# Kernel optimization log

Measured on AMD Instinct MI355X. Metric: run time of the kernel, lower is better.

Reference implementation:

```python
import jax, jax.numpy as jnp
import numpy as np

N, C, H, W = 64, 128, 32, 32
EPS = 1e-5


def _layernorm_chw(x, w, b):
    # LayerNorm over normalized_shape=(C,H,W): last 3 dims
    mu = jnp.mean(x, axis=(1, 2, 3), keepdims=True)
    var = jnp.var(x, axis=(1, 2, 3), keepdims=True)
    return (x - mu) * jax.lax.rsqrt(var + EPS) * w[None] + b[None]


def _conv1x1(x, w, b):
    # x: [N,C,H,W], w: [Cout,Cin], b: [Cout]
    return jnp.einsum('oc,nchw->nohw', w, x) + b[None, :, None, None]


def setup_inputs() -> dict:
    key = jax.random.key(0)
    ks = jax.random.split(key, 12)
    d = {
        'query': jax.random.normal(ks[0], (N, C, H, W), jnp.float32),
        'key': jax.random.normal(ks[1], (N, C, H, W), jnp.float32),
        'value': jax.random.normal(ks[2], (N, C, H, W), jnp.float32),
        'ln1_w': jnp.ones((C, H, W), jnp.float32),
        'ln1_b': jnp.zeros((C, H, W), jnp.float32),
        'ln2_w': jnp.ones((C, H, W), jnp.float32),
        'ln2_b': jnp.zeros((C, H, W), jnp.float32),
        'ln3_w': jnp.ones((C, H, W), jnp.float32),
        'ln3_b': jnp.zeros((C, H, W), jnp.float32),
        'wq': jax.random.normal(ks[3], (C, C), jnp.float32) / np.sqrt(C),
        'bq': jnp.zeros((C,), jnp.float32),
        'wk': jax.random.normal(ks[4], (C, C), jnp.float32) / np.sqrt(C),
        'bk': jnp.zeros((C,), jnp.float32),
        'wv': jax.random.normal(ks[5], (C, C), jnp.float32) / np.sqrt(C),
        'bv': jnp.zeros((C,), jnp.float32),
    }
    return d


def reference(query, key, value, ln1_w, ln1_b, ln2_w, ln2_b, ln3_w, ln3_b,
              wq, bq, wk, bk, wv, bv):
    qn = _layernorm_chw(query, ln1_w, ln1_b)  # residual uses normalized query
    kn = _layernorm_chw(key, ln2_w, ln2_b)
    vn = _layernorm_chw(value, ln3_w, ln3_b)
    q = _conv1x1(qn, wq, bq).reshape(N, C, H * W)
    k = _conv1x1(kn, wk, bk).reshape(N, C, H * W)
    v = _conv1x1(vn, wv, bv).reshape(N, C, H * W)
    # attention[n,i,j] = sum_c k[n,c,i] q[n,c,j] / sqrt(C); softmax over i (dim=1)
    attn = jnp.einsum('nci,ncj->nij', k, q) / jnp.sqrt(jnp.float32(C))
    attn = jax.nn.softmax(attn, axis=1)
    out = jnp.einsum('nci,nij->ncj', v, attn).reshape(N, C, H, W)
    x = qn + out
    return x.reshape(N, -1)  # flatten(start_dim=1)
```

## Files before the change

kernel.cpp:

```cpp
#include <hip/hip_runtime.h>


#define NS 64
#define CD 128
#define SD 1024
#define MEL (CD*SD)
#define SCALE 0.08838834764831845f

typedef __attribute__((ext_vector_type(4))) float floatx4;
typedef __attribute__((ext_vector_type(8))) short short8;
typedef __attribute__((ext_vector_type(4))) short short4v;

typedef __attribute__((address_space(1))) const void global_cvoid;
typedef __attribute__((address_space(3))) void lds_void;

__device__ __forceinline__ void gl16(const void* g, void* l) {
  __builtin_amdgcn_global_load_lds((global_cvoid*)g, (lds_void*)l, 16, 0, 0);
}
__device__ __forceinline__ unsigned short f2bf(float f) {
  union { float f; unsigned int i; } v; v.f = f;
  unsigned int i = v.i;
  return (unsigned short)((i + 0x7fffu + ((i >> 16) & 1u)) >> 16);
}
__device__ __forceinline__ unsigned int pkbf(float lo, float hi) {
  unsigned int r;
  asm("v_cvt_pk_bf16_f32 %0, %1, %2" : "=v"(r) : "v"(lo), "v"(hi));
  return r;
}
__device__ __forceinline__ short8 ld8_bf16(const float* __restrict__ p) {
  floatx4 a = *(const floatx4*)p;
  floatx4 b = *(const floatx4*)(p + 4);
  short8 r;
  r[0] = (short)f2bf(a[0]); r[1] = (short)f2bf(a[1]);
  r[2] = (short)f2bf(a[2]); r[3] = (short)f2bf(a[3]);
  r[4] = (short)f2bf(b[0]); r[5] = (short)f2bf(b[1]);
  r[6] = (short)f2bf(b[2]); r[7] = (short)f2bf(b[3]);
  return r;
}
__device__ __forceinline__ floatx4 mfma16(short8 a, short8 b, floatx4 c) {
  return __builtin_amdgcn_mfma_f32_16x16x32_bf16(a, b, c, 0, 0, 0);
}

__global__ __launch_bounds__(256) void stats_kernel(
    const float* __restrict__ q, const float* __restrict__ k,
    const float* __restrict__ v, float* __restrict__ sums)
{
  int b = blockIdx.x;
  int tn = b >> 3, part = b & 7;
  int t = tn >> 6;
  const float* x = (t == 0 ? q : (t == 1 ? k : v))
                 + (size_t)(tn & 63) * MEL + part * (MEL / 8);
  float s1 = 0.f, s2 = 0.f;
#pragma unroll
  for (int it = 0; it < 16; ++it) {
    floatx4 u = *(const floatx4*)(x + it * 1024 + threadIdx.x * 4);
#pragma unroll
    for (int j = 0; j < 4; ++j) { float f = u[j]; s1 += f; s2 += f * f; }
  }
#pragma unroll
  for (int off = 32; off; off >>= 1) {
    s1 += __shfl_xor(s1, off, 64);
    s2 += __shfl_xor(s2, off, 64);
  }
  if ((threadIdx.x & 63) == 0) {
    atomicAdd(&sums[tn], s1);
    atomicAdd(&sums[192 + tn], s2);
  }
}

__global__ __launch_bounds__(512, 4) void proj_kernel(
  const float* __restrict__ k, const float* __restrict__ v,
  const float* __restrict__ l2w, const float* __restrict__ l2b,
  const float* __restrict__ l3w, const float* __restrict__ l3b,
  const float* __restrict__ wk, const float* __restrict__ bk,
  const float* __restrict__ wv, const float* __restrict__ bv,
  const float* __restrict__ sums,
  unsigned short* __restrict__ kT, unsigned short* __restrict__ vN)
{
  int n  = blockIdx.x, t = blockIdx.y, st = blockIdx.z;
  const float* x  = (t == 0 ? k : v) + (size_t)n * MEL;
  const float* lw = (t == 0 ? l2w : l3w);
  const float* lb = (t == 0 ? l2b : l3b);
  const float* W  = (t == 0 ? wk : wv);
  const float* Bs = (t == 0 ? bk : bv);

  float mu  = sums[(t + 1) * 64 + n] * (1.f / MEL);
  float var = sums[192 + (t + 1) * 64 + n] * (1.f / MEL) - mu * mu;
  float rs  = rsqrtf(var + 1e-5f);
  float a_ln = rs, b_ln = -mu * rs;

  __shared__ __align__(16) unsigned short Xt[128 * 136];

  int tid = threadIdx.x;
  int cb = tid & 15, sb = (tid >> 4) & 15, half = tid >> 8;
  int s0 = st * 128;

  unsigned int w32[8][2];
#pragma unroll
  for (int pr = 0; pr < 2; ++pr) {
    int c0 = cb * 8 + half * 4 + pr * 2;
    const float* xp0 = x  + (size_t)c0 * SD + s0 + sb * 8;
    const float* wp0 = lw + (size_t)c0 * SD + s0 + sb * 8;
    const float* bp0 = lb + (size_t)c0 * SD + s0 + sb * 8;
    float xv0[8], xv1[8], wv0[8], wv1[8], bv0[8], bv1[8];
    *(floatx4*)xv0 = *(const floatx4*)xp0;       *(floatx4*)(xv0+4) = *(const floatx4*)(xp0+4);
    *(floatx4*)xv1 = *(const floatx4*)(xp0+SD);  *(floatx4*)(xv1+4) = *(const floatx4*)(xp0+SD+4);
    *(floatx4*)wv0 = *(const floatx4*)wp0;       *(floatx4*)(wv0+4) = *(const floatx4*)(wp0+4);
    *(floatx4*)wv1 = *(const floatx4*)(wp0+SD);  *(floatx4*)(wv1+4) = *(const floatx4*)(wp0+SD+4);
    *(floatx4*)bv0 = *(const floatx4*)bp0;       *(floatx4*)(bv0+4) = *(const floatx4*)(bp0+4);
    *(floatx4*)bv1 = *(const floatx4*)(bp0+SD);  *(floatx4*)(bv1+4) = *(const floatx4*)(bp0+SD+4);
#pragma unroll
    for (int js = 0; js < 8; ++js) {
      unsigned int lo = f2bf((xv0[js] * a_ln + b_ln) * wv0[js] + bv0[js]);
      unsigned int hi = f2bf((xv1[js] * a_ln + b_ln) * wv1[js] + bv1[js]);
      w32[js][pr] = lo | (hi << 16);
    }
  }
#pragma unroll
  for (int js = 0; js < 8; ++js) {
    unsigned int* d = (unsigned int*)&Xt[(sb * 8 + js) * 136 + cb * 8 + half * 4];
    d[0] = w32[js][0]; d[1] = w32[js][1];
  }
  __syncthreads();

  int lane = tid & 63, w = tid >> 6;
  int quad = lane >> 4, l16 = lane & 15;

  short8 Af[4];
#pragma unroll
  for (int kk = 0; kk < 4; ++kk)
    Af[kk] = ld8_bf16(W + (w * 16 + l16) * CD + kk * 32 + quad * 8);

  floatx4 acc[8];
  floatx4 zz = {0.f, 0.f, 0.f, 0.f};
#pragma unroll
  for (int nb = 0; nb < 8; ++nb) acc[nb] = zz;
#pragma unroll
  for (int kk = 0; kk < 4; ++kk)
#pragma unroll
    for (int nb = 0; nb < 8; ++nb) {
      short8 Bf = *(const short8*)&Xt[(nb * 16 + l16) * 136 + kk * 32 + quad * 8];
      acc[nb] = mfma16(Af[kk], Bf, acc[nb]);
    }

  float bsv[4];
#pragma unroll
  for (int r = 0; r < 4; ++r) bsv[r] = Bs[w * 16 + quad * 4 + r];

  if (t == 0) {
#pragma unroll
    for (int nb = 0; nb < 8; ++nb) {
      short4v pk;
#pragma unroll
      for (int r = 0; r < 4; ++r) pk[r] = (short)f2bf(acc[nb][r] + bsv[r]);
      size_t g = (size_t)n * MEL + (size_t)(s0 + nb * 16 + l16) * CD + w * 16 + quad * 4;
      *(short4v*)(kT + g) = pk;
    }
  } else {
#pragma unroll
    for (int nb = 0; nb < 8; ++nb)
#pragma unroll
      for (int r = 0; r < 4; ++r) {
        size_t g = (size_t)n * MEL + (size_t)(w * 16 + quad * 4 + r) * SD + s0 + nb * 16 + l16;
        vN[g] = f2bf(acc[nb][r] + bsv[r]);
      }
  }
}

__device__ __forceinline__ void stage_tile(
    const unsigned short* __restrict__ kbase0,
    const unsigned short* __restrict__ vbase0,
    char* smem, int ti, int buf, int w, int lane)
{
  const unsigned short* kb = kbase0 + (size_t)ti * 64 * CD;
  char* KD = smem + buf * 16384;
  char* VD = smem + 32768 + buf * 16384;
#pragma unroll
  for (int it = 0; it < 4; ++it) {
    int nch = w * 256 + it * 64 + lane;
    int i = nch >> 4, cc = nch & 15;
    int csrc = (cc & 8) | ((cc & 7) ^ (i & 7));
    gl16(kb + i * CD + csrc * 8, KD + (w * 256 + it * 64) * 16);
  }
#pragma unroll
  for (int it = 0; it < 4; ++it) {
    int nch = w * 256 + it * 64 + lane;
    int c = nch >> 3, ci = nch & 7;
    int isrc = ci ^ (c & 7);
    gl16(vbase0 + (size_t)c * SD + ti * 64 + isrc * 8, VD + (w * 256 + it * 64) * 16);
  }
}

__global__ __launch_bounds__(256, 2) void attn_kernel(
  const float* __restrict__ qraw, const float* __restrict__ l1w,
  const float* __restrict__ l1b, const float* __restrict__ wq,
  const float* __restrict__ bq,
  const unsigned short* __restrict__ kT, const unsigned short* __restrict__ vN,
  const float* __restrict__ sums, float* __restrict__ out)
{
  int n = blockIdx.x, jt = blockIdx.y;
  int j0 = jt * 128;

  __shared__ __align__(16) char smem[65536];
  unsigned short* Xt = (unsigned short*)smem;

  int tid = threadIdx.x, lane = tid & 63, w = tid >> 6;
  int quad = lane >> 4, l16 = lane & 15;

  float mu  = sums[n] * (1.f / MEL);
  float var = sums[192 + n] * (1.f / MEL) - mu * mu;
  float rsd = rsqrtf(var + 1e-5f);
  float a_ln = rsd, b_ln = -mu * rsd;
  const float* qb = qraw + (size_t)n * MEL;

  {
    int cb = tid & 15, sb = tid >> 4;
    unsigned int w32[8][4];
#pragma unroll
    for (int pr = 0; pr < 4; ++pr) {
      int c0 = cb * 8 + pr * 2;
      const float* xp0 = qb  + (size_t)c0 * SD + j0 + sb * 8;
      const float* wp0 = l1w + (size_t)c0 * SD + j0 + sb * 8;
      const float* bp0 = l1b + (size_t)c0 * SD + j0 + sb * 8;
      float xv0[8], xv1[8], wv0[8], wv1[8], bv0[8], bv1[8];
      *(floatx4*)xv0 = *(const floatx4*)xp0;       *(floatx4*)(xv0+4) = *(const floatx4*)(xp0+4);
      *(floatx4*)xv1 = *(const floatx4*)(xp0+SD);  *(floatx4*)(xv1+4) = *(const floatx4*)(xp0+SD+4);
      *(floatx4*)wv0 = *(const floatx4*)wp0;       *(floatx4*)(wv0+4) = *(const floatx4*)(wp0+4);
      *(floatx4*)wv1 = *(const floatx4*)(wp0+SD);  *(floatx4*)(wv1+4) = *(const floatx4*)(wp0+SD+4);
      *(floatx4*)bv0 = *(const floatx4*)bp0;       *(floatx4*)(bv0+4) = *(const floatx4*)(bp0+4);
      *(floatx4*)bv1 = *(const floatx4*)(bp0+SD);  *(floatx4*)(bv1+4) = *(const floatx4*)(bp0+SD+4);
#pragma unroll
      for (int js = 0; js < 8; ++js) {
        unsigned int lo = f2bf((xv0[js] * a_ln + b_ln) * wv0[js] + bv0[js]);
        unsigned int hi = f2bf((xv1[js] * a_ln + b_ln) * wv1[js] + bv1[js]);
        w32[js][pr] = lo | (hi << 16);
      }
    }
#pragma unroll
    for (int js = 0; js < 8; ++js)
      *(floatx4*)&Xt[(sb * 8 + js) * 136 + cb * 8] = *(floatx4*)w32[js];
  }
  __syncthreads();

  floatx4 zz = {0.f, 0.f, 0.f, 0.f};
  {
    short8 Af[2][4];
#pragma unroll
    for (int mi = 0; mi < 2; ++mi)
#pragma unroll
      for (int kk = 0; kk < 4; ++kk)
        Af[mi][kk] = ld8_bf16(wq + ((w * 2 + mi) * 16 + l16) * CD + kk * 32 + quad * 8);
    floatx4 accq[2][8];
#pragma unroll
    for (int mi = 0; mi < 2; ++mi)
#pragma unroll
      for (int nb = 0; nb < 8; ++nb) accq[mi][nb] = zz;
#pragma unroll
    for (int kk = 0; kk < 4; ++kk)
#pragma unroll
      for (int nb = 0; nb < 8; ++nb) {
        short8 Bf = *(const short8*)&Xt[(nb * 16 + l16) * 136 + kk * 32 + quad * 8];
        accq[0][nb] = mfma16(Af[0][kk], Bf, accq[0][nb]);
        accq[1][nb] = mfma16(Af[1][kk], Bf, accq[1][nb]);
      }
    __syncthreads();
    float bqs[2][4];
#pragma unroll
    for (int mi = 0; mi < 2; ++mi)
#pragma unroll
      for (int r = 0; r < 4; ++r) bqs[mi][r] = bq[(w * 2 + mi) * 16 + quad * 4 + r];
#pragma unroll
    for (int mi = 0; mi < 2; ++mi)
#pragma unroll
      for (int nb = 0; nb < 8; ++nb) {
        short4v pk;
#pragma unroll
        for (int r = 0; r < 4; ++r) pk[r] = (short)f2bf(accq[mi][nb][r] + bqs[mi][r]);
        *(short4v*)&Xt[(nb * 16 + l16) * 136 + (w * 2 + mi) * 16 + quad * 4] = pk;
      }
  }
  __syncthreads();

  short8 Qf[2][4];
#pragma unroll
  for (int nt = 0; nt < 2; ++nt)
#pragma unroll
    for (int kk = 0; kk < 4; ++kk)
      Qf[nt][kk] = *(const short8*)&Xt[((w * 2 + nt) * 16 + l16) * 136 + kk * 32 + quad * 8];
  __syncthreads();

  floatx4 Oc[8][2];
#pragma unroll
  for (int mt = 0; mt < 8; ++mt) { Oc[mt][0] = zz; Oc[mt][1] = zz; }
  float lsum[2] = {0.f, 0.f};

  const unsigned short* kbase0 = kT + (size_t)n * MEL;
  const unsigned short* vbase0 = vN + (size_t)n * MEL;

  int idx0 = l16 + ((quad & 1) << 5);
  int idx1 = idx0 + 16;
  bool hiq = quad >= 2;

  stage_tile(kbase0, vbase0, smem, 0, 0, w, lane);

  for (int itile = 0; itile < 16; ++itile) {
    int buf = itile & 1;
    __syncthreads();
    if (itile < 15) stage_tile(kbase0, vbase0, smem, itile + 1, buf ^ 1, w, lane);

    const unsigned short* Ks = (const unsigned short*)(smem + buf * 16384);
    const unsigned short* Vs = (const unsigned short*)(smem + 32768 + buf * 16384);

    floatx4 Sa[4][2];
#pragma unroll
    for (int mt = 0; mt < 4; ++mt) { Sa[mt][0] = zz; Sa[mt][1] = zz; }
    __builtin_amdgcn_s_setprio(1);
#pragma unroll
    for (int kk = 0; kk < 4; ++kk)
#pragma unroll
      for (int mt = 0; mt < 4; ++mt) {
        short8 Kf = *(const short8*)&Ks[(mt * 16 + l16) * 128 + (((kk * 4 + quad) ^ (l16 & 7)) * 8)];
        Sa[mt][0] = mfma16(Kf, Qf[0][kk], Sa[mt][0]);
        Sa[mt][1] = mfma16(Kf, Qf[1][kk], Sa[mt][1]);
      }
    __builtin_amdgcn_s_setprio(0);

    unsigned int pp[2][4][2];
#pragma unroll
    for (int nt = 0; nt < 2; ++nt)
#pragma unroll
      for (int mt = 0; mt < 4; ++mt) {
        float p0 = __expf(Sa[mt][nt][0] * SCALE);
        float p1 = __expf(Sa[mt][nt][1] * SCALE);
        float p2 = __expf(Sa[mt][nt][2] * SCALE);
        float p3 = __expf(Sa[mt][nt][3] * SCALE);
        lsum[nt] += (p0 + p1) + (p2 + p3);
        pp[nt][mt][0] = pkbf(p0, p1);
        pp[nt][mt][1] = pkbf(p2, p3);
      }

#pragma unroll
    for (int kk = 0; kk < 2; ++kk) {
      short8 Pf[2];
#pragma unroll
      for (int nt = 0; nt < 2; ++nt) {
        unsigned int d0a = (unsigned int)__shfl((int)pp[nt][2*kk  ][0], idx0, 64);
        unsigned int d0b = (unsigned int)__shfl((int)pp[nt][2*kk+1][0], idx0, 64);
        unsigned int d1a = (unsigned int)__shfl((int)pp[nt][2*kk  ][1], idx0, 64);
        unsigned int d1b = (unsigned int)__shfl((int)pp[nt][2*kk+1][1], idx0, 64);
        unsigned int d2a = (unsigned int)__shfl((int)pp[nt][2*kk  ][0], idx1, 64);
        unsigned int d2b = (unsigned int)__shfl((int)pp[nt][2*kk+1][0], idx1, 64);
        unsigned int d3a = (unsigned int)__shfl((int)pp[nt][2*kk  ][1], idx1, 64);
        unsigned int d3b = (unsigned int)__shfl((int)pp[nt][2*kk+1][1], idx1, 64);
        union { unsigned int u[4]; short8 s; } pu;
        pu.u[0] = hiq ? d0b : d0a;
        pu.u[1] = hiq ? d1b : d1a;
        pu.u[2] = hiq ? d2b : d2a;
        pu.u[3] = hiq ? d3b : d3a;
        Pf[nt] = pu.s;
      }
      __builtin_amdgcn_s_setprio(1);
#pragma unroll
      for (int mt = 0; mt < 8; ++mt) {
        short8 Vf = *(const short8*)&Vs[(mt * 16 + l16) * 64 + (((kk * 4 + quad) ^ (l16 & 7)) * 8)];
        Oc[mt][0] = mfma16(Vf, Pf[0], Oc[mt][0]);
        Oc[mt][1] = mfma16(Vf, Pf[1], Oc[mt][1]);
      }
      __builtin_amdgcn_s_setprio(0);
    }
  }

#pragma unroll
  for (int nt = 0; nt < 2; ++nt) {
    lsum[nt] += __shfl_xor(lsum[nt], 16, 64);
    lsum[nt] += __shfl_xor(lsum[nt], 32, 64);
  }
  float linv0 = 1.f / lsum[0], linv1 = 1.f / lsum[1];
  int jA = (w * 2) * 16 + l16, jB = jA + 16;

#pragma unroll
  for (int mt = 0; mt < 8; ++mt) {
#pragma unroll
    for (int r = 0; r < 4; ++r) {
      int c = mt * 16 + quad * 4 + r;
      const float* qp = qb  + (size_t)c * SD + j0;
      const float* wp = l1w + (size_t)c * SD + j0;
      const float* bp = l1b + (size_t)c * SD + j0;
      float* op = out + (size_t)n * MEL + (size_t)c * SD + j0;
      float qnA = (qp[jA] * a_ln + b_ln) * wp[jA] + bp[jA];
      float qnB = (qp[jB] * a_ln + b_ln) * wp[jB] + bp[jB];
      op[jA] = Oc[mt][0][r] * linv0 + qnA;
      op[jB] = Oc[mt][1][r] * linv1 + qnB;
    }
  }
}

extern "C" void kernel_launch(void* const* d_in, const int* in_sizes, int n_in,
                              void* d_out, int out_size, void* d_ws, size_t ws_size,
                              hipStream_t stream)
{
  const float* q   = (const float*)d_in[0];
  const float* k   = (const float*)d_in[1];
  const float* v   = (const float*)d_in[2];
  const float* l1w = (const float*)d_in[3];
  const float* l1b = (const float*)d_in[4];
  const float* l2w = (const float*)d_in[5];
  const float* l2b = (const float*)d_in[6];
  const float* l3w = (const float*)d_in[7];
  const float* l3b = (const float*)d_in[8];
  const float* wq  = (const float*)d_in[9];
  const float* bq  = (const float*)d_in[10];
  const float* wk  = (const float*)d_in[11];
  const float* bk  = (const float*)d_in[12];
  const float* wv  = (const float*)d_in[13];
  const float* bv  = (const float*)d_in[14];

  char* ws = (char*)d_ws;
  float* sums = (float*)ws;
  unsigned short* kT = (unsigned short*)(ws + 4096);
  unsigned short* vN = kT + (size_t)NS * MEL;

  hipMemsetAsync(sums, 0, 384 * sizeof(float), stream);
  stats_kernel<<<1536, 256, 0, stream>>>(q, k, v, sums);
  proj_kernel<<<dim3(64, 2, 8), 512, 0, stream>>>(k, v, l2w, l2b, l3w, l3b,
      wk, bk, wv, bv, sums, kT, vN);
  attn_kernel<<<dim3(64, 8), 256, 0, stream>>>(q, l1w, l1b, wq, bq, kT, vN,
      sums, (float*)d_out);
}
```

Before: 268.5 us.

## Drop memset via partial-sum stats, stage projection stores in LDS, tighten attention sync

The stats kernel now uses 512-thread blocks covering half a sample each. Each block reduces through shared memory and writes its partial sums to separate slots, so the atomics and the hipMemsetAsync are gone. The projection kernel transposes its bf16 output through LDS so global stores become coalesced 16-byte writes, which matters most for the strided V layout. The attention loop replaces __syncthreads with explicit vmcnt/lgkmcnt waits and raw barriers so the next tile's prefetch overlaps compute. It also reorders the accumulator array. The partial vmcnt(8) count depends on how many loads stage_tile issues and is a correctness risk if that assumption is wrong.

After: 259.3 us. -3.4%, faster.

```diff
diff --git a/kernel.cpp b/kernel.cpp
--- a/kernel.cpp
+++ b/kernel.cpp
@@ -41,19 +41,19 @@
   return __builtin_amdgcn_mfma_f32_16x16x32_bf16(a, b, c, 0, 0, 0);
 }
 
-__global__ __launch_bounds__(256) void stats_kernel(
+__global__ __launch_bounds__(512) void stats_kernel(
     const float* __restrict__ q, const float* __restrict__ k,
     const float* __restrict__ v, float* __restrict__ sums)
 {
   int b = blockIdx.x;
-  int tn = b >> 3, part = b & 7;
+  int tn = b >> 1, part = b & 1;
   int t = tn >> 6;
   const float* x = (t == 0 ? q : (t == 1 ? k : v))
-                 + (size_t)(tn & 63) * MEL + part * (MEL / 8);
+                 + (size_t)(tn & 63) * MEL + part * (MEL / 2);
   float s1 = 0.f, s2 = 0.f;
 #pragma unroll
-  for (int it = 0; it < 16; ++it) {
-    floatx4 u = *(const floatx4*)(x + it * 1024 + threadIdx.x * 4);
+  for (int it = 0; it < 32; ++it) {
+    floatx4 u = *(const floatx4*)(x + it * 2048 + threadIdx.x * 4);
 #pragma unroll
     for (int j = 0; j < 4; ++j) { float f = u[j]; s1 += f; s2 += f * f; }
   }
@@ -62,9 +62,16 @@
     s1 += __shfl_xor(s1, off, 64);
     s2 += __shfl_xor(s2, off, 64);
   }
-  if ((threadIdx.x & 63) == 0) {
-    atomicAdd(&sums[tn], s1);
-    atomicAdd(&sums[192 + tn], s2);
+  __shared__ float r1[8], r2[8];
+  int w = threadIdx.x >> 6;
+  if ((threadIdx.x & 63) == 0) { r1[w] = s1; r2[w] = s2; }
+  __syncthreads();
+  if (threadIdx.x == 0) {
+    float a = 0.f, c = 0.f;
+#pragma unroll
+    for (int i = 0; i < 8; ++i) { a += r1[i]; c += r2[i]; }
+    sums[part * 192 + tn] = a;
+    sums[384 + part * 192 + tn] = c;
   }
 }
 
@@ -84,8 +91,11 @@
   const float* W  = (t == 0 ? wk : wv);
   const float* Bs = (t == 0 ? bk : bv);
 
-  float mu  = sums[(t + 1) * 64 + n] * (1.f / MEL);
-  float var = sums[192 + (t + 1) * 64 + n] * (1.f / MEL) - mu * mu;
+  int tnS = (t + 1) * 64 + n;
+  float s1 = sums[tnS] + sums[192 + tnS];
+  float s2 = sums[384 + tnS] + sums[576 + tnS];
+  float mu  = s1 * (1.f / MEL);
+  float var = s2 * (1.f / MEL) - mu * mu;
   float rs  = rsqrtf(var + 1e-5f);
   float a_ln = rs, b_ln = -mu * rs;
 
@@ -147,23 +157,37 @@
 #pragma unroll
   for (int r = 0; r < 4; ++r) bsv[r] = Bs[w * 16 + quad * 4 + r];
 
-  if (t == 0) {
-#pragma unroll
-    for (int nb = 0; nb < 8; ++nb) {
-      short4v pk;
-#pragma unroll
-      for (int r = 0; r < 4; ++r) pk[r] = (short)f2bf(acc[nb][r] + bsv[r]);
-      size_t g = (size_t)n * MEL + (size_t)(s0 + nb * 16 + l16) * CD + w * 16 + quad * 4;
-      *(short4v*)(kT + g) = pk;
-    }
-  } else {
-#pragma unroll
-    for (int nb = 0; nb < 8; ++nb)
-#pragma unroll
-      for (int r = 0; r < 4; ++r) {
-        size_t g = (size_t)n * MEL + (size_t)(w * 16 + quad * 4 + r) * SD + s0 + nb * 16 + l16;
-        vN[g] = f2bf(acc[nb][r] + bsv[r]);
-      }
+  __syncthreads();
+  unsigned short* Ot = Xt;
+#pragma unroll
+  for (int nb = 0; nb < 8; ++nb) {
+    unsigned short pk[4];
+#pragma unroll
+    for (int r = 0; r < 4; ++r) pk[r] = f2bf(acc[nb][r] + bsv[r]);
+    unsigned int lo = (unsigned int)pk[0] | ((unsigned int)pk[1] << 16);
+    unsigned int hi = (unsigned int)pk[2] | ((unsigned int)pk[3] << 16);
+    if (t == 0) {
+      unsigned int* d = (unsigned int*)&Ot[(nb * 16 + l16) * 130 + w * 16 + quad * 4];
+      d[0] = lo; d[1] = hi;
+    } else {
+      int sl = nb * 16 + l16;
+#pragma unroll
+      for (int r = 0; r < 4; ++r)
+        Ot[(w * 16 + quad * 4 + r) * 130 + sl] = pk[r];
+    }
+  }
+  __syncthreads();
+  unsigned short* gbase = (t == 0) ? (kT + (size_t)n * MEL + (size_t)s0 * CD)
+                                   : (vN + (size_t)n * MEL + s0);
+#pragma unroll
+  for (int p = 0; p < 4; ++p) {
+    int g = p * 512 + tid;
+    int row = g >> 4, chunk = g & 15;
+    short8 val = *(const short8*)&Ot[row * 130 + chunk * 8];
+    if (t == 0)
+      *(short8*)(gbase + (size_t)row * CD + chunk * 8) = val;
+    else
+      *(short8*)(gbase + (size_t)row * SD + chunk * 8) = val;
   }
 }
 
@@ -207,8 +231,10 @@
   int tid = threadIdx.x, lane = tid & 63, w = tid >> 6;
   int quad = lane >> 4, l16 = lane & 15;
 
-  float mu  = sums[n] * (1.f / MEL);
-  float var = sums[192 + n] * (1.f / MEL) - mu * mu;
+  float s1 = sums[n] + sums[192 + n];
+  float s2 = sums[384 + n] + sums[576 + n];
+  float mu  = s1 * (1.f / MEL);
+  float var = s2 * (1.f / MEL) - mu * mu;
   float rsd = rsqrtf(var + 1e-5f);
   float a_ln = rsd, b_ln = -mu * rsd;
   const float* qb = qraw + (size_t)n * MEL;
@@ -289,9 +315,11 @@
       Qf[nt][kk] = *(const short8*)&Xt[((w * 2 + nt) * 16 + l16) * 136 + kk * 32 + quad * 8];
   __syncthreads();
 
-  floatx4 Oc[8][2];
-#pragma unroll
-  for (int mt = 0; mt < 8; ++mt) { Oc[mt][0] = zz; Oc[mt][1] = zz; }
+  floatx4 Oc[2][8];
+#pragma unroll
+  for (int mi = 0; mi < 2; ++mi)
+#pragma unroll
+    for (int nb = 0; nb < 8; ++nb) Oc[mi][nb] = zz;
   float lsum[2] = {0.f, 0.f};
 
   const unsigned short* kbase0 = kT + (size_t)n * MEL;
@@ -305,8 +333,14 @@
 
   for (int itile = 0; itile < 16; ++itile) {
     int buf = itile & 1;
-    __syncthreads();
-    if (itile < 15) stage_tile(kbase0, vbase0, smem, itile + 1, buf ^ 1, w, lane);
+    if (itile < 15) {
+      stage_tile(kbase0, vbase0, smem, itile + 1, buf ^ 1, w, lane);
+      asm volatile("s_waitcnt vmcnt(8)" ::: "memory");
+    } else {
+      asm volatile("s_waitcnt vmcnt(0)" ::: "memory");
+    }
+    __builtin_amdgcn_s_barrier();
+    __builtin_amdgcn_sched_barrier(0);
 
     const unsigned short* Ks = (const unsigned short*)(smem + buf * 16384);
     const unsigned short* Vs = (const unsigned short*)(smem + 32768 + buf * 16384);
@@ -363,11 +397,15 @@
 #pragma unroll
       for (int mt = 0; mt < 8; ++mt) {
         short8 Vf = *(const short8*)&Vs[(mt * 16 + l16) * 64 + (((kk * 4 + quad) ^ (l16 & 7)) * 8)];
-        Oc[mt][0] = mfma16(Vf, Pf[0], Oc[mt][0]);
-        Oc[mt][1] = mfma16(Vf, Pf[1], Oc[mt][1]);
+        Oc[0][mt] = mfma16(Vf, Pf[0], Oc[0][mt]);
+        Oc[1][mt] = mfma16(Vf, Pf[1], Oc[1][mt]);
       }
       __builtin_amdgcn_s_setprio(0);
     }
+
+    asm volatile("s_waitcnt lgkmcnt(0)" ::: "memory");
+    __builtin_amdgcn_s_barrier();
+    __builtin_amdgcn_sched_barrier(0);
   }
 
 #pragma unroll
@@ -389,8 +427,8 @@
       float* op = out + (size_t)n * MEL + (size_t)c * SD + j0;
       float qnA = (qp[jA] * a_ln + b_ln) * wp[jA] + bp[jA];
       float qnB = (qp[jB] * a_ln + b_ln) * wp[jB] + bp[jB];
-      op[jA] = Oc[mt][0][r] * linv0 + qnA;
-      op[jB] = Oc[mt][1][r] * linv1 + qnB;
+      op[jA] = Oc[0][mt][r] * linv0 + qnA;
+      op[jB] = Oc[1][mt][r] * linv1 + qnB;
     }
   }
 }
@@ -420,8 +458,7 @@
   unsigned short* kT = (unsigned short*)(ws + 4096);
   unsigned short* vN = kT + (size_t)NS * MEL;
 
-  hipMemsetAsync(sums, 0, 384 * sizeof(float), stream);
-  stats_kernel<<<1536, 256, 0, stream>>>(q, k, v, sums);
+  stats_kernel<<<384, 512, 0, stream>>>(q, k, v, sums);
   proj_kernel<<<dim3(64, 2, 8), 512, 0, stream>>>(k, v, l2w, l2b, l3w, l3b,
       wk, bk, wv, bv, sums, kT, vN);
   attn_kernel<<<dim3(64, 8), 256, 0, stream>>>(q, l1w, l1b, wq, bq, kT, vN,
```
